# Performance work log

Measured on AMD Instinct MI355X. Metric: run time of the kernel, lower is better.

Reference implementation:

```python
import jax, jax.numpy as jnp
import numpy as np

B, T, S, E, H = 4, 2048, 2048, 512, 8
D = E // H  # head_dim = 64
BIFURCATION_FACTOR = 1.0


def setup_inputs() -> dict:
    key = jax.random.key(0)
    ks = jax.random.split(key, 12)
    s = 1.0 / np.sqrt(E)
    return {
        "query": jax.random.normal(ks[0], (B, T, E), jnp.float32),
        "key_": jax.random.normal(ks[1], (B, S, E), jnp.float32),
        "value": jax.random.normal(ks[2], (B, S, E), jnp.float32),
        "Wq": jax.random.uniform(ks[3], (E, E), jnp.float32, -s, s),
        "bq": jax.random.uniform(ks[4], (E,), jnp.float32, -s, s),
        "Wk": jax.random.uniform(ks[5], (E, E), jnp.float32, -s, s),
        "bk": jax.random.uniform(ks[6], (E,), jnp.float32, -s, s),
        "Wv": jax.random.uniform(ks[7], (E, E), jnp.float32, -s, s),
        "bv": jax.random.uniform(ks[8], (E,), jnp.float32, -s, s),
        "Wo": jax.random.uniform(ks[9], (E, E), jnp.float32, -s, s),
        "bo": jax.random.uniform(ks[10], (E,), jnp.float32, -s, s),
        "r": jnp.asarray(3.5, jnp.float32),
    }


def _logistic_map(x, r):
    # sigmoid-normalize then one logistic-map iteration with learned r
    xn = jax.nn.sigmoid(x)
    r_scaled = BIFURCATION_FACTOR * jax.nn.sigmoid(r) * 4.0
    return r_scaled * xn * (1.0 - xn)


def reference(query, key_, value, Wq, bq, Wk, bk, Wv, bv, Wo, bo, r):
    q = _logistic_map(query @ Wq.T + bq, r)   # [B,T,E]
    k = _logistic_map(key_ @ Wk.T + bk, r)    # [B,S,E]
    v = value @ Wv.T + bv                     # [B,S,E]

    q = q.reshape(B, T, H, D).transpose(0, 2, 1, 3)  # [B,H,T,D]
    k = k.reshape(B, S, H, D).transpose(0, 2, 1, 3)  # [B,H,S,D]
    v = v.reshape(B, S, H, D).transpose(0, 2, 1, 3)  # [B,H,S,D]

    scores = jnp.einsum('bhtd,bhsd->bhts', q, k) / jnp.sqrt(jnp.asarray(D, q.dtype))
    attn = jax.nn.softmax(scores, axis=-1)           # [B,H,T,S]
    out = jnp.einsum('bhts,bhsd->bhtd', attn, v)     # [B,H,T,D]
    out = out.transpose(0, 2, 1, 3).reshape(B, T, E)
    return out @ Wo.T + bo
```

## Files before the change

kernel.cpp:

```cpp
#include <hip/hip_runtime.h>
#include <stdint.h>

#define B_ 4
#define T_ 2048
#define S_ 2048
#define E_ 512
#define H_ 8
#define D_ 64

using bf16x8 = __attribute__((ext_vector_type(8))) short;
using bf16x4 = __attribute__((ext_vector_type(4))) short;
using f32x4  = __attribute__((ext_vector_type(4))) float;

__device__ __forceinline__ unsigned short f2bf(float f) {
  unsigned u = __float_as_uint(f);
  u += 0x7fffu + ((u >> 16) & 1u);
  return (unsigned short)(u >> 16);
}

__device__ __forceinline__ float sigmoidf_(float x) {
  return 1.0f / (1.0f + __expf(-x));
}

__device__ __forceinline__ f32x4 mfma16x16x16(bf16x4 a, bf16x4 b, f32x4 c) {
#if __has_builtin(__builtin_amdgcn_mfma_f32_16x16x16bf16_1k)
  return __builtin_amdgcn_mfma_f32_16x16x16bf16_1k(a, b, c, 0, 0, 0);
#else
  asm("v_mfma_f32_16x16x16_bf16 %0, %1, %2, %0" : "+v"(c) : "v"(a), "v"(b));
  return c;
#endif
}

__device__ __forceinline__ void gl16(const void* g, void* l) {
  __builtin_amdgcn_global_load_lds(
      (const __attribute__((address_space(1))) unsigned*)g,
      (__attribute__((address_space(3))) unsigned*)l,
      16, 0, 0);
}

__device__ __forceinline__ int swzi(int row, int ebyte) {
  return row * 64 + ((ebyte ^ ((row & 7) << 4)) >> 1);
}

__global__ __launch_bounds__(256) void cvt3_bf16(
    const float* __restrict__ a, const float* __restrict__ b, const float* __restrict__ c,
    unsigned short* __restrict__ oa, unsigned short* __restrict__ ob,
    unsigned short* __restrict__ oc, int n4) {
  int seg = blockIdx.x >> 9;
  const float* in = (seg == 0) ? a : (seg == 1) ? b : c;
  unsigned short* out = (seg == 0) ? oa : (seg == 1) ? ob : oc;
  int i = (blockIdx.x & 511) * 256 + threadIdx.x;
  for (; i < n4; i += 512 * 256) {
    float4 v = ((const float4*)in)[i];
    ushort4 o;
    o.x = f2bf(v.x); o.y = f2bf(v.y); o.z = f2bf(v.z); o.w = f2bf(v.w);
    ((ushort4*)out)[i] = o;
  }
}

__global__ __launch_bounds__(256) void cvt4_bf16(
    const float* __restrict__ a, const float* __restrict__ b,
    const float* __restrict__ c, const float* __restrict__ d,
    unsigned short* __restrict__ oa, unsigned short* __restrict__ ob,
    unsigned short* __restrict__ oc, unsigned short* __restrict__ od, int n4) {
  int seg = blockIdx.x >> 7;
  const float* in = (seg == 0) ? a : (seg == 1) ? b : (seg == 2) ? c : d;
  unsigned short* out = (seg == 0) ? oa : (seg == 1) ? ob : (seg == 2) ? oc : od;
  int i = (blockIdx.x & 127) * 256 + threadIdx.x;
  for (; i < n4; i += 128 * 256) {
    float4 v = ((const float4*)in)[i];
    ushort4 o;
    o.x = f2bf(v.x); o.y = f2bf(v.y); o.z = f2bf(v.z); o.w = f2bf(v.w);
    ((ushort4*)out)[i] = o;
  }
}

__global__ __launch_bounds__(256) void gemm_out(
    const unsigned short* __restrict__ A,
    const unsigned short* __restrict__ W,
    const float* __restrict__ bias,
    float* __restrict__ outp) {
  __shared__ unsigned short As[2][128 * 64];
  __shared__ unsigned short Bs[2][64 * 64];

  int bid = ((blockIdx.x & 7) << 6) + (blockIdx.x >> 3);
  int tid = threadIdx.x;
  int lane = tid & 63, wid = tid >> 6;
  int bm = bid >> 3, bn = bid & 7;
  int m0 = bm * 128, n0 = bn * 64;

  f32x4 acc[4][2] = {};

  int rowc = tid >> 3;
  int kswz = ((tid & 7) ^ (rowc & 7)) << 4;

  auto stage = [&](int buf, int kt) {
#pragma unroll
    for (int c = 0; c < 4; ++c) {
      const char* ga = (const char*)A + (size_t)(m0 + c * 32 + rowc) * 1024 + kt * 128 + kswz;
      gl16(ga, (char*)&As[buf][0] + c * 4096 + (wid << 10));
    }
#pragma unroll
    for (int c = 0; c < 2; ++c) {
      const char* gw = (const char*)W + (size_t)(n0 + c * 32 + rowc) * 1024 + kt * 128 + kswz;
      gl16(gw, (char*)&Bs[buf][0] + c * 4096 + (wid << 10));
    }
  };

  stage(0, 0);

  int wm = wid >> 1, wn = wid & 1;
  int fr = lane & 15, fg = lane >> 4;

  for (int kt = 0; kt < 8; ++kt) {
    __syncthreads();
    if (kt < 7) stage((kt + 1) & 1, kt + 1);
    int buf = kt & 1;
#pragma unroll
    for (int ks = 0; ks < 2; ++ks) {
      bf16x8 a[4], b[2];
#pragma unroll
      for (int mi = 0; mi < 4; ++mi)
        a[mi] = *(const bf16x8*)&As[buf][swzi(wm * 64 + mi * 16 + fr, ks * 64 + fg * 16)];
#pragma unroll
      for (int ni = 0; ni < 2; ++ni)
        b[ni] = *(const bf16x8*)&Bs[buf][swzi(wn * 32 + ni * 16 + fr, ks * 64 + fg * 16)];
#pragma unroll
      for (int mi = 0; mi < 4; ++mi)
#pragma unroll
        for (int ni = 0; ni < 2; ++ni)
          acc[mi][ni] = __builtin_amdgcn_mfma_f32_16x16x32_bf16(a[mi], b[ni], acc[mi][ni], 0, 0, 0);
    }
  }

#pragma unroll
  for (int mi = 0; mi < 4; ++mi)
#pragma unroll
    for (int ni = 0; ni < 2; ++ni)
#pragma unroll
      for (int i = 0; i < 4; ++i) {
        int gm = m0 + wm * 64 + mi * 16 + fg * 4 + i;
        int gn = n0 + wn * 32 + ni * 16 + fr;
        outp[(size_t)gm * E_ + gn] = acc[mi][ni][i] + bias[gn];
      }
}

__global__ __launch_bounds__(256) void gemm_proj(
    const unsigned short* __restrict__ Aq, const unsigned short* __restrict__ Wqp,
    const float* __restrict__ bqp, unsigned short* __restrict__ oq,
    const unsigned short* __restrict__ Ak, const unsigned short* __restrict__ Wkp,
    const float* __restrict__ bkp, unsigned short* __restrict__ ok,
    const unsigned short* __restrict__ Av, const unsigned short* __restrict__ Wvp,
    const float* __restrict__ bvp, unsigned short* __restrict__ ov,
    const float* __restrict__ rptr, float sclq) {
  __shared__ unsigned short As[2][128 * 64];
  __shared__ unsigned short Bs[2][64 * 64];

  int job = blockIdx.x >> 9;
  int x = blockIdx.x & 511;
  int bid = ((x & 7) << 6) + (x >> 3);
  const unsigned short* A = (job == 0) ? Aq : (job == 1) ? Ak : Av;
  const unsigned short* W = (job == 0) ? Wqp : (job == 1) ? Wkp : Wvp;
  const float* bias = (job == 0) ? bqp : (job == 1) ? bkp : bvp;
  unsigned short* outp = (job == 0) ? oq : (job == 1) ? ok : ov;

  int bm, bn;
  if (job == 2) { bm = bid >> 7; bn = bid & 127; }
  else          { bm = bid >> 3; bn = bid & 7; }
  int m0 = bm * 128, n0 = bn * 64;

  f32x4 acc[4][2] = {};

  int tid = threadIdx.x;
  int lane = tid & 63, wid = tid >> 6;
  int rowc = tid >> 3;
  int kswz = ((tid & 7) ^ (rowc & 7)) << 4;

  auto stage = [&](int buf, int kt) {
#pragma unroll
    for (int c = 0; c < 4; ++c) {
      const char* ga = (const char*)A + (size_t)(m0 + c * 32 + rowc) * 1024 + kt * 128 + kswz;
      gl16(ga, (char*)&As[buf][0] + c * 4096 + (wid << 10));
    }
#pragma unroll
    for (int c = 0; c < 2; ++c) {
      const char* gw = (const char*)W + (size_t)(n0 + c * 32 + rowc) * 1024 + kt * 128 + kswz;
      gl16(gw, (char*)&Bs[buf][0] + c * 4096 + (wid << 10));
    }
  };

  stage(0, 0);

  int wm = wid >> 1, wn = wid & 1;
  int fr = lane & 15, fg = lane >> 4;

  for (int kt = 0; kt < 8; ++kt) {
    __syncthreads();
    if (kt < 7) stage((kt + 1) & 1, kt + 1);
    int buf = kt & 1;
#pragma unroll
    for (int ks = 0; ks < 2; ++ks) {
      bf16x8 a[4], b[2];
#pragma unroll
      for (int mi = 0; mi < 4; ++mi)
        a[mi] = *(const bf16x8*)&As[buf][swzi(wm * 64 + mi * 16 + fr, ks * 64 + fg * 16)];
#pragma unroll
      for (int ni = 0; ni < 2; ++ni)
        b[ni] = *(const bf16x8*)&Bs[buf][swzi(wn * 32 + ni * 16 + fr, ks * 64 + fg * 16)];
#pragma unroll
      for (int mi = 0; mi < 4; ++mi)
#pragma unroll
        for (int ni = 0; ni < 2; ++ni)
          acc[mi][ni] = __builtin_amdgcn_mfma_f32_16x16x32_bf16(a[mi], b[ni], acc[mi][ni], 0, 0, 0);
    }
  }

  float rs = 4.0f * sigmoidf_(rptr[0]) * ((job == 0) ? sclq : 1.0f);

#pragma unroll
  for (int mi = 0; mi < 4; ++mi) {
#pragma unroll
    for (int ni = 0; ni < 2; ++ni) {
#pragma unroll
      for (int i = 0; i < 4; ++i) {
        int gm = m0 + wm * 64 + mi * 16 + fg * 4 + i;
        int gn = n0 + wn * 32 + ni * 16 + fr;
        float v = acc[mi][ni][i];
        if (job < 2) {
          v += bias[gn];
          float xn = sigmoidf_(v);
          float val = rs * xn * (1.0f - xn);
          int b = gm >> 11, t = gm & 2047, h = gn >> 6, d = gn & 63;
          outp[((size_t)(b * H_ + h) * T_ + t) * D_ + d] = f2bf(val);
        } else {
          v += bias[gm];
          int h = gm >> 6, d = gm & 63, b = gn >> 11, s = gn & 2047;
          outp[((size_t)(b * H_ + h) * D_ + d) * S_ + s] = f2bf(v);
        }
      }
    }
  }
}

template <int CBa, int CBb>
__device__ __forceinline__ void tile_pair(
    char* sm, int koff0, int koff1, const int (&voff)[4],
    const bf16x8 (&qa)[2][2], f32x4 (&acco)[2][4], float (&lst)[2]) {
  union PU { unsigned u[2]; bf16x4 v; };

  bf16x8 ka[4][2];
#pragma unroll
  for (int ni = 0; ni < 4; ++ni) {
    ka[ni][0] = *(const bf16x8*)(sm + CBa + ni * 2048 + koff0);
    ka[ni][1] = *(const bf16x8*)(sm + CBa + ni * 2048 + koff1);
  }
  f32x4 sta[4][2] = {};
  __builtin_amdgcn_s_setprio(1);
#pragma unroll
  for (int ni = 0; ni < 4; ++ni)
#pragma unroll
    for (int mi = 0; mi < 2; ++mi) {
      sta[ni][mi] = __builtin_amdgcn_mfma_f32_16x16x32_bf16(ka[ni][0], qa[mi][0], sta[ni][mi], 0, 0, 0);
      sta[ni][mi] = __builtin_amdgcn_mfma_f32_16x16x32_bf16(ka[ni][1], qa[mi][1], sta[ni][mi], 0, 0, 0);
    }
  __builtin_amdgcn_s_setprio(0);

  bf16x8 kb[4][2];
#pragma unroll
  for (int ni = 0; ni < 4; ++ni) {
    kb[ni][0] = *(const bf16x8*)(sm + CBb + ni * 2048 + koff0);
    kb[ni][1] = *(const bf16x8*)(sm + CBb + ni * 2048 + koff1);
  }
  f32x4 stb[4][2] = {};
  __builtin_amdgcn_s_setprio(1);
#pragma unroll
  for (int ni = 0; ni < 4; ++ni)
#pragma unroll
    for (int mi = 0; mi < 2; ++mi) {
      stb[ni][mi] = __builtin_amdgcn_mfma_f32_16x16x32_bf16(kb[ni][0], qa[mi][0], stb[ni][mi], 0, 0, 0);
      stb[ni][mi] = __builtin_amdgcn_mfma_f32_16x16x32_bf16(kb[ni][1], qa[mi][1], stb[ni][mi], 0, 0, 0);
    }
  __builtin_amdgcn_s_setprio(0);

  bf16x4 pfa[2][4];
#pragma unroll
  for (int mi = 0; mi < 2; ++mi) {
    float sum = 0.f;
#pragma unroll
    for (int ni = 0; ni < 4; ++ni) {
      float p0 = __builtin_amdgcn_exp2f(sta[ni][mi][0]);
      float p1 = __builtin_amdgcn_exp2f(sta[ni][mi][1]);
      float p2 = __builtin_amdgcn_exp2f(sta[ni][mi][2]);
      float p3 = __builtin_amdgcn_exp2f(sta[ni][mi][3]);
      sum += (p0 + p1) + (p2 + p3);
      PU pu;
      asm("v_cvt_pk_bf16_f32 %0, %1, %2" : "=v"(pu.u[0]) : "v"(p0), "v"(p1));
      asm("v_cvt_pk_bf16_f32 %0, %1, %2" : "=v"(pu.u[1]) : "v"(p2), "v"(p3));
      pfa[mi][ni] = pu.v;
    }
    sum += __shfl_xor(sum, 16);
    sum += __shfl_xor(sum, 32);
    lst[mi] += sum;
  }

  __builtin_amdgcn_s_setprio(1);
#pragma unroll
  for (int nd = 0; nd < 4; ++nd)
#pragma unroll
    for (int ni = 0; ni < 4; ++ni) {
      bf16x4 vf = *(const bf16x4*)(sm + CBa + nd * 2048 + voff[ni]);
#pragma unroll
      for (int mi = 0; mi < 2; ++mi)
        acco[mi][nd] = mfma16x16x16(vf, pfa[mi][ni], acco[mi][nd]);
    }
  __builtin_amdgcn_s_setprio(0);

  bf16x4 pfb[2][4];
#pragma unroll
  for (int mi = 0; mi < 2; ++mi) {
    float sum = 0.f;
#pragma unroll
    for (int ni = 0; ni < 4; ++ni) {
      float p0 = __builtin_amdgcn_exp2f(stb[ni][mi][0]);
      float p1 = __builtin_amdgcn_exp2f(stb[ni][mi][1]);
      float p2 = __builtin_amdgcn_exp2f(stb[ni][mi][2]);
      float p3 = __builtin_amdgcn_exp2f(stb[ni][mi][3]);
      sum += (p0 + p1) + (p2 + p3);
      PU pu;
      asm("v_cvt_pk_bf16_f32 %0, %1, %2" : "=v"(pu.u[0]) : "v"(p0), "v"(p1));
      asm("v_cvt_pk_bf16_f32 %0, %1, %2" : "=v"(pu.u[1]) : "v"(p2), "v"(p3));
      pfb[mi][ni] = pu.v;
    }
    sum += __shfl_xor(sum, 16);
    sum += __shfl_xor(sum, 32);
    lst[mi] += sum;
  }

  __builtin_amdgcn_s_setprio(1);
#pragma unroll
  for (int nd = 0; nd < 4; ++nd)
#pragma unroll
    for (int ni = 0; ni < 4; ++ni) {
      bf16x4 vf = *(const bf16x4*)(sm + CBb + nd * 2048 + voff[ni]);
#pragma unroll
      for (int mi = 0; mi < 2; ++mi)
        acco[mi][nd] = mfma16x16x16(vf, pfb[mi][ni], acco[mi][nd]);
    }
  __builtin_amdgcn_s_setprio(0);
}

__global__ __launch_bounds__(256) void attn_flash(
    const unsigned short* __restrict__ qp,
    const unsigned short* __restrict__ kp,
    const unsigned short* __restrict__ vtp,
    unsigned short* __restrict__ attno) {
  __shared__ __align__(16) char smem[65536];

  int tid = threadIdx.x, lane = tid & 63, wid = tid >> 6;
  int wgid = ((blockIdx.x & 7) << 6) + (blockIdx.x >> 3);
  int tt = wgid & 15, bh = wgid >> 4;
  const char* qh = (const char*)qp + ((size_t)bh * T_ + tt * 128) * 128;
  const char* kh = (const char*)kp + (size_t)bh * S_ * 128;
  const char* vh = (const char*)vtp + (size_t)bh * D_ * S_ * 2;

  int rowc = tid >> 3;
  int kswz = ((tid & 7) ^ (rowc & 7)) << 4;

#define STAGE_K(SB, IT) { \
    gl16(kh + (size_t)((IT) * 64 + rowc) * 128 + kswz, smem + (SB) + (wid << 10)); \
    gl16(kh + (size_t)((IT) * 64 + 32 + rowc) * 128 + kswz, smem + (SB) + 4096 + (wid << 10)); }
#define STAGE_V(SB, IT) { \
    gl16(vh + (size_t)rowc * 4096 + (IT) * 128 + kswz, smem + (SB) + 8192 + (wid << 10)); \
    gl16(vh + (size_t)(32 + rowc) * 4096 + (IT) * 128 + kswz, smem + (SB) + 12288 + (wid << 10)); }

  STAGE_K(0, 0) STAGE_V(0, 0) STAGE_K(16384, 1) STAGE_V(16384, 1)
#pragma unroll
  for (int c = 0; c < 4; ++c)
    gl16(qh + (size_t)(c * 32 + rowc) * 128 + kswz, smem + 49152 + c * 4096 + (wid << 10));

  int fr = lane & 15, fg = (lane >> 4) & 3;
  int qrb = wid * 32;
  int koff0 = fr * 128 + ((fg * 16) ^ ((fr & 7) << 4));
  int koff1 = fr * 128 + ((64 + fg * 16) ^ ((fr & 7) << 4));
  int voff[4];
#pragma unroll
  for (int ni = 0; ni < 4; ++ni)
    voff[ni] = 8192 + fr * 128 + ((ni * 32 + fg * 8) ^ ((fr & 7) << 4));

  __syncthreads();

  bf16x8 qa[2][2];
#pragma unroll
  for (int mi = 0; mi < 2; ++mi) {
    qa[mi][0] = *(const bf16x8*)(smem + 49152 + (qrb + mi * 16) * 128 + koff0);
    qa[mi][1] = *(const bf16x8*)(smem + 49152 + (qrb + mi * 16) * 128 + koff1);
  }
  __syncthreads();

  f32x4 acco[2][4] = {};
  float lst[2] = {0.f, 0.f};

  STAGE_K(32768, 2) STAGE_V(32768, 2) STAGE_K(49152, 3) STAGE_V(49152, 3)
  tile_pair<0, 16384>(smem, koff0, koff1, voff, qa, acco, lst);

#pragma unroll 1
  for (int pp = 1; pp <= 7; ++pp) {
    int ta = pp * 4;
    __syncthreads();
    STAGE_K(0, ta) STAGE_V(0, ta) STAGE_K(16384, ta + 1) STAGE_V(16384, ta + 1)
    tile_pair<32768, 49152>(smem, koff0, koff1, voff, qa, acco, lst);
    __syncthreads();
    STAGE_K(32768, ta + 2) STAGE_V(32768, ta + 2) STAGE_K(49152, ta + 3) STAGE_V(49152, ta + 3)
    tile_pair<0, 16384>(smem, koff0, koff1, voff, qa, acco, lst);
  }
  __syncthreads();
  tile_pair<32768, 49152>(smem, koff0, koff1, voff, qa, acco, lst);

  int b = bh >> 3, h = bh & 7;
#pragma unroll
  for (int mi = 0; mi < 2; ++mi) {
    float rl = 1.0f / lst[mi];
    int t = tt * 128 + qrb + mi * 16 + fr;
    unsigned short* rowp = attno + (size_t)(b * T_ + t) * E_ + h * 64;
#pragma unroll
    for (int nd = 0; nd < 4; ++nd) {
      ushort4 o;
      o.x = f2bf(acco[mi][nd][0] * rl);
      o.y = f2bf(acco[mi][nd][1] * rl);
      o.z = f2bf(acco[mi][nd][2] * rl);
      o.w = f2bf(acco[mi][nd][3] * rl);
      *(ushort4*)(rowp + nd * 16 + fg * 4) = o;
    }
  }
#undef STAGE_K
#undef STAGE_V
}

extern "C" void kernel_launch(void* const* d_in, const int* in_sizes, int n_in,
                              void* d_out, int out_size, void* d_ws, size_t ws_size,
                              hipStream_t stream) {
  const float* query = (const float*)d_in[0];
  const float* key_  = (const float*)d_in[1];
  const float* value = (const float*)d_in[2];
  const float* Wq    = (const float*)d_in[3];
  const float* bq    = (const float*)d_in[4];
  const float* Wk    = (const float*)d_in[5];
  const float* bk    = (const float*)d_in[6];
  const float* Wv    = (const float*)d_in[7];
  const float* bv    = (const float*)d_in[8];
  const float* Wo    = (const float*)d_in[9];
  const float* bo    = (const float*)d_in[10];
  const float* r     = (const float*)d_in[11];

  char* ws = (char*)d_ws;
  unsigned short* qb    = (unsigned short*)(ws + 0);
  unsigned short* kb    = (unsigned short*)(ws + 8388608);
  unsigned short* vb    = (unsigned short*)(ws + 16777216);
  unsigned short* wqb   = (unsigned short*)(ws + 25165824);
  unsigned short* wkb   = (unsigned short*)(ws + 25690112);
  unsigned short* wvb   = (unsigned short*)(ws + 26214400);
  unsigned short* wob   = (unsigned short*)(ws + 26738688);
  unsigned short* qp    = (unsigned short*)(ws + 27262976);
  unsigned short* kp    = (unsigned short*)(ws + 35651584);
  unsigned short* vtp   = (unsigned short*)(ws + 44040192);
  unsigned short* attno = (unsigned short*)(ws + 52428800);

  cvt3_bf16<<<1536, 256, 0, stream>>>(query, key_, value, qb, kb, vb, (B_ * T_ * E_) / 4);
  cvt4_bf16<<<512, 256, 0, stream>>>(Wq, Wk, Wv, Wo, wqb, wkb, wvb, wob, (E_ * E_) / 4);

  const float SCLQ = 0.125f * 1.44269504089f;

  gemm_proj<<<1536, 256, 0, stream>>>(qb, wqb, bq, qp,
                                      kb, wkb, bk, kp,
                                      wvb, vb, bv, vtp, r, SCLQ);

  attn_flash<<<512, 256, 0, stream>>>(qp, kp, vtp, attno);

  gemm_out<<<512, 256, 0, stream>>>(attno, wob, bo, (float*)d_out);
}
```

Before: 114.5 us.

## Split attention across two KV halves with a separate combine kernel

Each attention block now processes only half of the key/value sequence, doubling the grid to 1024 blocks, and writes unnormalized fp32 partial outputs and row sums. A new combine kernel adds the two partials, normalizes, and writes bf16 output. Shared memory drops from 64KB to 32KB with a two-buffer pipeline of single tiles, which could raise occupancy. The cost is extra fp32 global traffic of about 32MB written and read, plus one more launch. Scratch buffers reuse the output array and freed workspace regions.

```diff
diff --git a/kernel.cpp b/kernel.cpp
--- a/kernel.cpp
+++ b/kernel.cpp
@@ -242,61 +242,48 @@
   }
 }
 
-template <int CBa, int CBb>
-__device__ __forceinline__ void tile_pair(
+template <int CB>
+__device__ __forceinline__ void tile_step(
     char* sm, int koff0, int koff1, const int (&voff)[4],
     const bf16x8 (&qa)[2][2], f32x4 (&acco)[2][4], float (&lst)[2]) {
+  bf16x8 kb[4][2];
+#pragma unroll
+  for (int ni = 0; ni < 4; ++ni) {
+    kb[ni][0] = *(const bf16x8*)(sm + CB + ni * 2048 + koff0);
+    kb[ni][1] = *(const bf16x8*)(sm + CB + ni * 2048 + koff1);
+  }
+  f32x4 st[4][2];
+#pragma unroll
+  for (int ni = 0; ni < 4; ++ni)
+#pragma unroll
+    for (int mi = 0; mi < 2; ++mi) st[ni][mi] = f32x4{0.f, 0.f, 0.f, 0.f};
+
+  __builtin_amdgcn_s_setprio(1);
+#pragma unroll
+  for (int ni = 0; ni < 4; ++ni)
+#pragma unroll
+    for (int mi = 0; mi < 2; ++mi) {
+      st[ni][mi] = __builtin_amdgcn_mfma_f32_16x16x32_bf16(kb[ni][0], qa[mi][0], st[ni][mi], 0, 0, 0);
+      st[ni][mi] = __builtin_amdgcn_mfma_f32_16x16x32_bf16(kb[ni][1], qa[mi][1], st[ni][mi], 0, 0, 0);
+    }
+  __builtin_amdgcn_s_setprio(0);
+
   union PU { unsigned u[2]; bf16x4 v; };
-
-  bf16x8 ka[4][2];
-#pragma unroll
-  for (int ni = 0; ni < 4; ++ni) {
-    ka[ni][0] = *(const bf16x8*)(sm + CBa + ni * 2048 + koff0);
-    ka[ni][1] = *(const bf16x8*)(sm + CBa + ni * 2048 + koff1);
-  }
-  f32x4 sta[4][2] = {};
-  __builtin_amdgcn_s_setprio(1);
-#pragma unroll
-  for (int ni = 0; ni < 4; ++ni)
-#pragma unroll
-    for (int mi = 0; mi < 2; ++mi) {
-      sta[ni][mi] = __builtin_amdgcn_mfma_f32_16x16x32_bf16(ka[ni][0], qa[mi][0], sta[ni][mi], 0, 0, 0);
-      sta[ni][mi] = __builtin_amdgcn_mfma_f32_16x16x32_bf16(ka[ni][1], qa[mi][1], sta[ni][mi], 0, 0, 0);
-    }
-  __builtin_amdgcn_s_setprio(0);
-
-  bf16x8 kb[4][2];
-#pragma unroll
-  for (int ni = 0; ni < 4; ++ni) {
-    kb[ni][0] = *(const bf16x8*)(sm + CBb + ni * 2048 + koff0);
-    kb[ni][1] = *(const bf16x8*)(sm + CBb + ni * 2048 + koff1);
-  }
-  f32x4 stb[4][2] = {};
-  __builtin_amdgcn_s_setprio(1);
-#pragma unroll
-  for (int ni = 0; ni < 4; ++ni)
-#pragma unroll
-    for (int mi = 0; mi < 2; ++mi) {
-      stb[ni][mi] = __builtin_amdgcn_mfma_f32_16x16x32_bf16(kb[ni][0], qa[mi][0], stb[ni][mi], 0, 0, 0);
-      stb[ni][mi] = __builtin_amdgcn_mfma_f32_16x16x32_bf16(kb[ni][1], qa[mi][1], stb[ni][mi], 0, 0, 0);
-    }
-  __builtin_amdgcn_s_setprio(0);
-
-  bf16x4 pfa[2][4];
+  bf16x4 pfr[2][4];
 #pragma unroll
   for (int mi = 0; mi < 2; ++mi) {
     float sum = 0.f;
 #pragma unroll
     for (int ni = 0; ni < 4; ++ni) {
-      float p0 = __builtin_amdgcn_exp2f(sta[ni][mi][0]);
-      float p1 = __builtin_amdgcn_exp2f(sta[ni][mi][1]);
-      float p2 = __builtin_amdgcn_exp2f(sta[ni][mi][2]);
-      float p3 = __builtin_amdgcn_exp2f(sta[ni][mi][3]);
+      float p0 = __builtin_amdgcn_exp2f(st[ni][mi][0]);
+      float p1 = __builtin_amdgcn_exp2f(st[ni][mi][1]);
+      float p2 = __builtin_amdgcn_exp2f(st[ni][mi][2]);
+      float p3 = __builtin_amdgcn_exp2f(st[ni][mi][3]);
       sum += (p0 + p1) + (p2 + p3);
       PU pu;
       asm("v_cvt_pk_bf16_f32 %0, %1, %2" : "=v"(pu.u[0]) : "v"(p0), "v"(p1));
       asm("v_cvt_pk_bf16_f32 %0, %1, %2" : "=v"(pu.u[1]) : "v"(p2), "v"(p3));
-      pfa[mi][ni] = pu.v;
+      pfr[mi][ni] = pu.v;
     }
     sum += __shfl_xor(sum, 16);
     sum += __shfl_xor(sum, 32);
@@ -308,60 +295,28 @@
   for (int nd = 0; nd < 4; ++nd)
 #pragma unroll
     for (int ni = 0; ni < 4; ++ni) {
-      bf16x4 vf = *(const bf16x4*)(sm + CBa + nd * 2048 + voff[ni]);
+      bf16x4 vf = *(const bf16x4*)(sm + CB + nd * 2048 + voff[ni]);
 #pragma unroll
       for (int mi = 0; mi < 2; ++mi)
-        acco[mi][nd] = mfma16x16x16(vf, pfa[mi][ni], acco[mi][nd]);
+        acco[mi][nd] = mfma16x16x16(vf, pfr[mi][ni], acco[mi][nd]);
     }
   __builtin_amdgcn_s_setprio(0);
-
-  bf16x4 pfb[2][4];
-#pragma unroll
-  for (int mi = 0; mi < 2; ++mi) {
-    float sum = 0.f;
-#pragma unroll
-    for (int ni = 0; ni < 4; ++ni) {
-      float p0 = __builtin_amdgcn_exp2f(stb[ni][mi][0]);
-      float p1 = __builtin_amdgcn_exp2f(stb[ni][mi][1]);
-      float p2 = __builtin_amdgcn_exp2f(stb[ni][mi][2]);
-      float p3 = __builtin_amdgcn_exp2f(stb[ni][mi][3]);
-      sum += (p0 + p1) + (p2 + p3);
-      PU pu;
-      asm("v_cvt_pk_bf16_f32 %0, %1, %2" : "=v"(pu.u[0]) : "v"(p0), "v"(p1));
-      asm("v_cvt_pk_bf16_f32 %0, %1, %2" : "=v"(pu.u[1]) : "v"(p2), "v"(p3));
-      pfb[mi][ni] = pu.v;
-    }
-    sum += __shfl_xor(sum, 16);
-    sum += __shfl_xor(sum, 32);
-    lst[mi] += sum;
-  }
-
-  __builtin_amdgcn_s_setprio(1);
-#pragma unroll
-  for (int nd = 0; nd < 4; ++nd)
-#pragma unroll
-    for (int ni = 0; ni < 4; ++ni) {
-      bf16x4 vf = *(const bf16x4*)(sm + CBb + nd * 2048 + voff[ni]);
-#pragma unroll
-      for (int mi = 0; mi < 2; ++mi)
-        acco[mi][nd] = mfma16x16x16(vf, pfb[mi][ni], acco[mi][nd]);
-    }
-  __builtin_amdgcn_s_setprio(0);
-}
-
-__global__ __launch_bounds__(256) void attn_flash(
+}
+
+__global__ __launch_bounds__(256) void attn_split(
     const unsigned short* __restrict__ qp,
     const unsigned short* __restrict__ kp,
     const unsigned short* __restrict__ vtp,
-    unsigned short* __restrict__ attno) {
-  __shared__ __align__(16) char smem[65536];
+    float* __restrict__ O0, float* __restrict__ O1,
+    float* __restrict__ l0, float* __restrict__ l1) {
+  __shared__ __align__(16) char smem[32768];
 
   int tid = threadIdx.x, lane = tid & 63, wid = tid >> 6;
-  int wgid = ((blockIdx.x & 7) << 6) + (blockIdx.x >> 3);
-  int tt = wgid & 15, bh = wgid >> 4;
+  int wgid = ((blockIdx.x & 7) << 7) + (blockIdx.x >> 3);
+  int sh = wgid & 1, tt = (wgid >> 1) & 15, bh = wgid >> 5;
   const char* qh = (const char*)qp + ((size_t)bh * T_ + tt * 128) * 128;
-  const char* kh = (const char*)kp + (size_t)bh * S_ * 128;
-  const char* vh = (const char*)vtp + (size_t)bh * D_ * S_ * 2;
+  const char* kh = (const char*)kp + (size_t)bh * S_ * 128 + (size_t)sh * 1024 * 128;
+  const char* vh = (const char*)vtp + (size_t)bh * D_ * S_ * 2 + sh * 2048;
 
   int rowc = tid >> 3;
   int kswz = ((tid & 7) ^ (rowc & 7)) << 4;
@@ -373,10 +328,10 @@
     gl16(vh + (size_t)rowc * 4096 + (IT) * 128 + kswz, smem + (SB) + 8192 + (wid << 10)); \
     gl16(vh + (size_t)(32 + rowc) * 4096 + (IT) * 128 + kswz, smem + (SB) + 12288 + (wid << 10)); }
 
-  STAGE_K(0, 0) STAGE_V(0, 0) STAGE_K(16384, 1) STAGE_V(16384, 1)
+  STAGE_K(0, 0) STAGE_V(0, 0)
 #pragma unroll
   for (int c = 0; c < 4; ++c)
-    gl16(qh + (size_t)(c * 32 + rowc) * 128 + kswz, smem + 49152 + c * 4096 + (wid << 10));
+    gl16(qh + (size_t)(c * 32 + rowc) * 128 + kswz, smem + 16384 + c * 4096 + (wid << 10));
 
   int fr = lane & 15, fg = (lane >> 4) & 3;
   int qrb = wid * 32;
@@ -392,48 +347,67 @@
   bf16x8 qa[2][2];
 #pragma unroll
   for (int mi = 0; mi < 2; ++mi) {
-    qa[mi][0] = *(const bf16x8*)(smem + 49152 + (qrb + mi * 16) * 128 + koff0);
-    qa[mi][1] = *(const bf16x8*)(smem + 49152 + (qrb + mi * 16) * 128 + koff1);
+    qa[mi][0] = *(const bf16x8*)(smem + 16384 + (qrb + mi * 16) * 128 + koff0);
+    qa[mi][1] = *(const bf16x8*)(smem + 16384 + (qrb + mi * 16) * 128 + koff1);
   }
   __syncthreads();
 
   f32x4 acco[2][4] = {};
   float lst[2] = {0.f, 0.f};
 
-  STAGE_K(32768, 2) STAGE_V(32768, 2) STAGE_K(49152, 3) STAGE_V(49152, 3)
-  tile_pair<0, 16384>(smem, koff0, koff1, voff, qa, acco, lst);
+  STAGE_K(16384, 1) STAGE_V(16384, 1)
+  tile_step<0>(smem, koff0, koff1, voff, qa, acco, lst);
 
 #pragma unroll 1
-  for (int pp = 1; pp <= 7; ++pp) {
-    int ta = pp * 4;
+  for (int pp = 0; pp <= 6; ++pp) {
+    int ta = pp * 2;
     __syncthreads();
-    STAGE_K(0, ta) STAGE_V(0, ta) STAGE_K(16384, ta + 1) STAGE_V(16384, ta + 1)
-    tile_pair<32768, 49152>(smem, koff0, koff1, voff, qa, acco, lst);
+    STAGE_K(0, ta + 2) STAGE_V(0, ta + 2)
+    tile_step<16384>(smem, koff0, koff1, voff, qa, acco, lst);
     __syncthreads();
-    STAGE_K(32768, ta + 2) STAGE_V(32768, ta + 2) STAGE_K(49152, ta + 3) STAGE_V(49152, ta + 3)
-    tile_pair<0, 16384>(smem, koff0, koff1, voff, qa, acco, lst);
+    STAGE_K(16384, ta + 3) STAGE_V(16384, ta + 3)
+    tile_step<0>(smem, koff0, koff1, voff, qa, acco, lst);
   }
   __syncthreads();
-  tile_pair<32768, 49152>(smem, koff0, koff1, voff, qa, acco, lst);
-
+  tile_step<16384>(smem, koff0, koff1, voff, qa, acco, lst);
+
+  float* Op = sh ? O1 : O0;
+  float* lp = sh ? l1 : l0;
   int b = bh >> 3, h = bh & 7;
 #pragma unroll
   for (int mi = 0; mi < 2; ++mi) {
-    float rl = 1.0f / lst[mi];
     int t = tt * 128 + qrb + mi * 16 + fr;
-    unsigned short* rowp = attno + (size_t)(b * T_ + t) * E_ + h * 64;
-#pragma unroll
-    for (int nd = 0; nd < 4; ++nd) {
-      ushort4 o;
-      o.x = f2bf(acco[mi][nd][0] * rl);
-      o.y = f2bf(acco[mi][nd][1] * rl);
-      o.z = f2bf(acco[mi][nd][2] * rl);
-      o.w = f2bf(acco[mi][nd][3] * rl);
-      *(ushort4*)(rowp + nd * 16 + fg * 4) = o;
-    }
+    float* rowp = Op + (size_t)(b * T_ + t) * E_ + h * 64;
+#pragma unroll
+    for (int nd = 0; nd < 4; ++nd)
+      *(f32x4*)(rowp + nd * 16 + fg * 4) = acco[mi][nd];
+    if (lane < 16)
+      lp[bh * 2048 + t] = lst[mi];
   }
 #undef STAGE_K
 #undef STAGE_V
+}
+
+__global__ __launch_bounds__(256) void combine_o(
+    const float* __restrict__ O0, const float* __restrict__ O1,
+    const float* __restrict__ l0, const float* __restrict__ l1,
+    unsigned short* __restrict__ attno) {
+  const int n4 = (B_ * T_ * E_) / 4;
+  for (int i4 = blockIdx.x * 256 + threadIdx.x; i4 < n4; i4 += gridDim.x * 256) {
+    int i = i4 << 2;
+    int row = i >> 9;
+    int h = (i & 511) >> 6;
+    int li = ((row >> 11) * H_ + h) * 2048 + (row & 2047);
+    float4 a = ((const float4*)O0)[i4];
+    float4 c = ((const float4*)O1)[i4];
+    float rl = 1.0f / (l0[li] + l1[li]);
+    ushort4 o;
+    o.x = f2bf((a.x + c.x) * rl);
+    o.y = f2bf((a.y + c.y) * rl);
+    o.z = f2bf((a.z + c.z) * rl);
+    o.w = f2bf((a.w + c.w) * rl);
+    ((ushort4*)attno)[i4] = o;
+  }
 }
 
 extern "C" void kernel_launch(void* const* d_in, const int* in_sizes, int n_in,
@@ -465,6 +439,11 @@
   unsigned short* vtp   = (unsigned short*)(ws + 44040192);
   unsigned short* attno = (unsigned short*)(ws + 52428800);
 
+  float* O0 = (float*)d_out;
+  float* O1 = (float*)(ws + 0);
+  float* l0 = (float*)(ws + 16777216);
+  float* l1 = (float*)(ws + 17039360);
+
   cvt3_bf16<<<1536, 256, 0, stream>>>(query, key_, value, qb, kb, vb, (B_ * T_ * E_) / 4);
   cvt4_bf16<<<512, 256, 0, stream>>>(Wq, Wk, Wv, Wo, wqb, wkb, wvb, wob, (E_ * E_) / 4);
 
@@ -474,7 +453,8 @@
                                       kb, wkb, bk, kp,
                                       wvb, vb, bv, vtp, r, SCLQ);
 
-  attn_flash<<<512, 256, 0, stream>>>(qp, kp, vtp, attno);
+  attn_split<<<1024, 256, 0, stream>>>(qp, kp, vtp, O0, O1, l0, l1);
+  combine_o<<<2048, 256, 0, stream>>>(O0, O1, l0, l1, attno);
 
   gemm_out<<<512, 256, 0, stream>>>(attno, wob, bo, (float*)d_out);
 }
```

Result: slower. 125.5 us (+9.6%).
